# Optimization experiments

Hardware: AMD Instinct MI355X
Metric: run time of the kernel (lower is better)

## Reference

```python
import jax, jax.numpy as jnp
import numpy as np

K = 5            # kernel_size for gaussian and bilateral
PAD = K // 2
SIGMA = 1.0          # gaussian sigma / bilateral sigma_spatial
SIGMA_INT = 0.1      # bilateral sigma_intensity


def _spatial_kernel():
    coords = jnp.arange(K, dtype=jnp.float32) - K // 2
    x, y = jnp.meshgrid(coords, coords, indexing='ij')
    return jnp.exp(-(x ** 2 + y ** 2) / (2.0 * SIGMA ** 2))  # (K, K), unnormalized


def setup_inputs() -> dict:
    key = jax.random.key(0)
    images = jax.random.uniform(key, (8, 3, 512, 512), dtype=jnp.float32)
    return {"images": images}


def _gaussian_filter(images):
    g = _spatial_kernel()
    g = g / g.sum()
    kernel = jnp.tile(g[None, None], (3, 1, 1, 1))  # (3,1,K,K) depthwise
    return jax.lax.conv_general_dilated(
        images, kernel, window_strides=(1, 1),
        padding=[(PAD, PAD), (PAD, PAD)],
        dimension_numbers=('NCHW', 'OIHW', 'NCHW'),
        feature_group_count=3)


def _bilateral_filter(images):
    B, C, H, W = images.shape
    padded = jnp.pad(images, ((0, 0), (0, 0), (PAD, PAD), (PAD, PAD)), mode='reflect')
    # im2col: (B, C, K*K, H, W) -- fixed 25-iteration loop over kernel offsets
    patches = jnp.stack([padded[:, :, i:i + H, j:j + W]
                         for i in range(K) for j in range(K)], axis=2)
    center = patches[:, :, K * K // 2:K * K // 2 + 1]  # (B,C,1,H,W)
    iw = jnp.exp(-(patches - center) ** 2 / (2.0 * SIGMA_INT ** 2))
    sw = _spatial_kernel().reshape(1, 1, K * K, 1, 1)
    w = sw * iw
    w = w / (w.sum(axis=2, keepdims=True) + 1e-8)
    return (patches * w).sum(axis=2)  # (B,C,H,W)


def reference(images):
    # AdaptiveAntiAlias.forward(images, mode='auto')
    gaussian_out = _gaussian_filter(images)
    bilateral_out = _bilateral_filter(images)
    return 0.6 * gaussian_out + 0.4 * bilateral_out
```

## Files before the change

kernel.cpp:

```cpp
#include <hip/hip_runtime.h>

#define IMG_H 512
#define IMG_W 512
#define NCH   24

#if __has_builtin(__builtin_amdgcn_exp2f)
#define EXP2(x) __builtin_amdgcn_exp2f(x)
#else
#define EXP2(x) exp2f(x)
#endif
#if __has_builtin(__builtin_amdgcn_rcpf)
#define RCP(x) __builtin_amdgcn_rcpf(x)
#else
#define RCP(x) (1.0f/(x))
#endif

__device__ __forceinline__ double exs(int r2) {
    switch (r2) {
        case 0: return 1.0;
        case 1: return 0.60653065971263342;
        case 2: return 0.36787944117144233;
        case 4: return 0.13533528323661270;
        case 5: return 0.08208499862389880;
        case 8: return 0.01831563888873418;
    }
    return 0.0;
}

#define SSUM 6.16892408102888092
#define NEG50_LOG2E -72.134752044448169f
#define NEGHALF_LOG2E -0.72134752044448169f

#define XG_INT 126
#define YR_INT 508
#define PER_CH_INT (XG_INT * YR_INT)
#define N_INT (PER_CH_INT * NCH)
#define PER_CH_B (4 * 128 + YR_INT * 2)
#define N_B (PER_CH_B * NCH)

__global__ __launch_bounds__(256) void aa_kernel(const float* __restrict__ in,
                                                 float* __restrict__ out) {
    const int gid = blockIdx.x * 256 + threadIdx.x;

    if (gid < N_INT) {
        const int ch  = gid / PER_CH_INT;
        const int rem = gid - ch * PER_CH_INT;
        const int yy  = rem / XG_INT;
        const int y   = 2 + yy;
        const int x0  = 4 + (rem - yy * XG_INT) * 4;

        const float* __restrict__ img = in + ch * (IMG_H * IMG_W);

        float v[5][8];
        const float* base = img + (y - 2) * IMG_W + (x0 - 2);
        #pragma unroll
        for (int r = 0; r < 5; ++r) {
            const float2* rp = (const float2*)(base + r * IMG_W);
            float2 a = rp[0], b = rp[1], c = rp[2], d = rp[3];
            v[r][0] = a.x; v[r][1] = a.y; v[r][2] = b.x; v[r][3] = b.y;
            v[r][4] = c.x; v[r][5] = c.y; v[r][6] = d.x; v[r][7] = d.y;
        }

        float res[4];
        #pragma unroll
        for (int p = 0; p < 4; ++p) {
            const float ctr = v[2][2 + p];
            float g = 0.f, wsum = 0.f, bsum = 0.f;
            #pragma unroll
            for (int i = 0; i < 5; ++i) {
                #pragma unroll
                for (int j = 0; j < 5; ++j) {
                    const int r2 = (i - 2) * (i - 2) + (j - 2) * (j - 2);
                    const float gk  = (float)(exs(r2) / SSUM);
                    const float lsw = NEGHALF_LOG2E * (float)r2;
                    const float val = v[i][p + j];
                    const float d   = val - ctr;
                    const float w   = EXP2(fmaf(d * d, NEG50_LOG2E, lsw));
                    wsum += w;
                    bsum = fmaf(w, val, bsum);
                    g    = fmaf(gk, val, g);
                }
            }
            res[p] = 0.6f * g + 0.4f * (bsum * RCP(wsum + 1e-8f));
        }

        float4* o4 = (float4*)(out + ch * (IMG_H * IMG_W) + y * IMG_W + x0);
        *o4 = make_float4(res[0], res[1], res[2], res[3]);
    } else {
        const int bi = gid - N_INT;
        const int ch = bi / PER_CH_B;
        const int r  = bi - ch * PER_CH_B;
        int y, x0;
        if (r < 512) {
            const int q = r >> 7;
            y  = (q < 2) ? q : q + 508;
            x0 = (r & 127) << 2;
        } else {
            const int r2_ = r - 512;
            y  = 2 + (r2_ >> 1);
            x0 = (r2_ & 1) ? (IMG_W - 4) : 0;
        }

        const float* __restrict__ img = in + ch * (IMG_H * IMG_W);

        float res[4];
        #pragma unroll
        for (int p = 0; p < 4; ++p) {
            const int x = x0 + p;
            const float ctr = img[y * IMG_W + x];
            float g = 0.f, wsum = 0.f, bsum = 0.f;
            #pragma unroll
            for (int i = 0; i < 5; ++i) {
                const int yy = y + i - 2;
                const bool yin = (yy >= 0) & (yy < IMG_H);
                const int ry = (yy < 0) ? -yy : ((yy >= IMG_H) ? 2 * IMG_H - 2 - yy : yy);
                #pragma unroll
                for (int j = 0; j < 5; ++j) {
                    const int r2 = (i - 2) * (i - 2) + (j - 2) * (j - 2);
                    const float gk  = (float)(exs(r2) / SSUM);
                    const float lsw = NEGHALF_LOG2E * (float)r2;
                    const int xx = x + j - 2;
                    const bool xin = (xx >= 0) & (xx < IMG_W);
                    const int rx = (xx < 0) ? -xx : ((xx >= IMG_W) ? 2 * IMG_W - 2 - xx : xx);
                    const float val = img[ry * IMG_W + rx];
                    const float d   = val - ctr;
                    const float w   = EXP2(fmaf(d * d, NEG50_LOG2E, lsw));
                    wsum += w;
                    bsum = fmaf(w, val, bsum);
                    if (yin & xin) g = fmaf(gk, val, g);
                }
            }
            res[p] = 0.6f * g + 0.4f * (bsum * RCP(wsum + 1e-8f));
        }

        float4* o4 = (float4*)(out + ch * (IMG_H * IMG_W) + y * IMG_W + x0);
        *o4 = make_float4(res[0], res[1], res[2], res[3]);
    }
}

extern "C" void kernel_launch(void* const* d_in, const int* in_sizes, int n_in,
                              void* d_out, int out_size, void* d_ws, size_t ws_size,
                              hipStream_t stream) {
    const float* img = (const float*)d_in[0];
    float* out = (float*)d_out;
    const int total = N_INT + N_B;
    aa_kernel<<<total / 256, 256, 0, stream>>>(img, out);
}
```

Before: 39.36 us.

## Compute two output rows per thread and make the Gaussian separable

Each interior thread now computes a 2x4 output tile from 6 loaded rows instead of a 1x4 tile from 5, so overlapping rows are loaded once and reused. The Gaussian part is split into a vertical column-sum pass and a 5-tap horizontal pass, which cuts its FMAs. The launch bounds also add a minimum-occupancy hint. In exchange, each thread holds more live registers and there are half as many interior threads, which may lower parallelism or cause register spills.

```diff
diff --git a/kernel.cpp b/kernel.cpp
--- a/kernel.cpp
+++ b/kernel.cpp
@@ -4,90 +4,119 @@
 #define IMG_W 512
 #define NCH   24
 
+__device__ __forceinline__ float fexp2(float x) {
 #if __has_builtin(__builtin_amdgcn_exp2f)
-#define EXP2(x) __builtin_amdgcn_exp2f(x)
+    return __builtin_amdgcn_exp2f(x);
 #else
-#define EXP2(x) exp2f(x)
+    float r; asm("v_exp_f32 %0, %1" : "=v"(r) : "v"(x)); return r;
 #endif
+}
+__device__ __forceinline__ float frcp(float x) {
 #if __has_builtin(__builtin_amdgcn_rcpf)
-#define RCP(x) __builtin_amdgcn_rcpf(x)
+    return __builtin_amdgcn_rcpf(x);
 #else
-#define RCP(x) (1.0f/(x))
+    float r; asm("v_rcp_f32 %0, %1" : "=v"(r) : "v"(x)); return r;
 #endif
-
-__device__ __forceinline__ double exs(int r2) {
-    switch (r2) {
-        case 0: return 1.0;
-        case 1: return 0.60653065971263342;
-        case 2: return 0.36787944117144233;
-        case 4: return 0.13533528323661270;
-        case 5: return 0.08208499862389880;
-        case 8: return 0.01831563888873418;
-    }
-    return 0.0;
 }
 
+__device__ __forceinline__ constexpr double exs(int r2) {
+    return (r2 == 0) ? 1.0
+         : (r2 == 1) ? 0.60653065971263342
+         : (r2 == 2) ? 0.36787944117144233
+         : (r2 == 4) ? 0.13533528323661270
+         : (r2 == 5) ? 0.08208499862389880
+         : (r2 == 8) ? 0.01831563888873418 : 0.0;
+}
 #define SSUM 6.16892408102888092
-#define NEG50_LOG2E -72.134752044448169f
-#define NEGHALF_LOG2E -0.72134752044448169f
+__device__ __forceinline__ constexpr float gkc(int r2) { return (float)(exs(r2) / SSUM); }
+__device__ __forceinline__ constexpr float k1(int d)  { return (float)exs(d * d); }
+__device__ __forceinline__ constexpr float k1n(int d) { return (float)(exs(d * d) / SSUM); }
+#define NEG50  -72.134752044448169f
+#define LG     -0.72134752044448169f
 
 #define XG_INT 126
-#define YR_INT 508
-#define PER_CH_INT (XG_INT * YR_INT)
-#define N_INT (PER_CH_INT * NCH)
-#define PER_CH_B (4 * 128 + YR_INT * 2)
+#define YT_INT 254
+#define PER_CH_T (XG_INT * YT_INT)
+#define N_INT (PER_CH_T * NCH)
+#define PER_CH_B (4 * 128 + 508 * 2)
 #define N_B (PER_CH_B * NCH)
+#define N_TOTAL (N_INT + N_B)
 
-__global__ __launch_bounds__(256) void aa_kernel(const float* __restrict__ in,
-                                                 float* __restrict__ out) {
+__global__ __launch_bounds__(256, 4) void aa_kernel(const float* __restrict__ in,
+                                                    float* __restrict__ out) {
     const int gid = blockIdx.x * 256 + threadIdx.x;
 
     if (gid < N_INT) {
-        const int ch  = gid / PER_CH_INT;
-        const int rem = gid - ch * PER_CH_INT;
-        const int yy  = rem / XG_INT;
-        const int y   = 2 + yy;
-        const int x0  = 4 + (rem - yy * XG_INT) * 4;
+        const int ch  = gid / PER_CH_T;
+        const int rem = gid - ch * PER_CH_T;
+        const int ty  = rem / XG_INT;
+        const int y0  = 2 + ty * 2;
+        const int x0  = 4 + (rem - ty * XG_INT) * 4;
 
         const float* __restrict__ img = in + ch * (IMG_H * IMG_W);
+        const float* base = img + (y0 - 2) * IMG_W + (x0 - 2);
 
-        float v[5][8];
-        const float* base = img + (y - 2) * IMG_W + (x0 - 2);
+        float2 L[6][4];
         #pragma unroll
-        for (int r = 0; r < 5; ++r) {
+        for (int r = 0; r < 6; ++r) {
             const float2* rp = (const float2*)(base + r * IMG_W);
-            float2 a = rp[0], b = rp[1], c = rp[2], d = rp[3];
-            v[r][0] = a.x; v[r][1] = a.y; v[r][2] = b.x; v[r][3] = b.y;
-            v[r][4] = c.x; v[r][5] = c.y; v[r][6] = d.x; v[r][7] = d.y;
+            #pragma unroll
+            for (int c = 0; c < 4; ++c) L[r][c] = rp[c];
+        }
+        #define V(r, c) (((c) & 1) ? L[r][(c) >> 1].y : L[r][(c) >> 1].x)
+
+        float cs[2][8];
+        #pragma unroll
+        for (int yr = 0; yr < 2; ++yr) {
+            #pragma unroll
+            for (int c = 0; c < 8; ++c) {
+                float s = k1(2) * V(yr + 0, c);
+                s = fmaf(k1(1), V(yr + 1, c), s);
+                s = fmaf(k1(0), V(yr + 2, c), s);
+                s = fmaf(k1(1), V(yr + 3, c), s);
+                s = fmaf(k1(2), V(yr + 4, c), s);
+                cs[yr][c] = s;
+            }
         }
 
-        float res[4];
+        float res[2][4];
         #pragma unroll
-        for (int p = 0; p < 4; ++p) {
-            const float ctr = v[2][2 + p];
-            float g = 0.f, wsum = 0.f, bsum = 0.f;
+        for (int yr = 0; yr < 2; ++yr) {
             #pragma unroll
-            for (int i = 0; i < 5; ++i) {
+            for (int p = 0; p < 4; ++p) {
+                const float ctr = V(2 + yr, 2 + p);
+                float wsum = 0.f, bsum = 0.f;
                 #pragma unroll
-                for (int j = 0; j < 5; ++j) {
-                    const int r2 = (i - 2) * (i - 2) + (j - 2) * (j - 2);
-                    const float gk  = (float)(exs(r2) / SSUM);
-                    const float lsw = NEGHALF_LOG2E * (float)r2;
-                    const float val = v[i][p + j];
-                    const float d   = val - ctr;
-                    const float w   = EXP2(fmaf(d * d, NEG50_LOG2E, lsw));
-                    wsum += w;
-                    bsum = fmaf(w, val, bsum);
-                    g    = fmaf(gk, val, g);
+                for (int i = 0; i < 5; ++i) {
+                    #pragma unroll
+                    for (int j = 0; j < 5; ++j) {
+                        const int r2 = (i - 2) * (i - 2) + (j - 2) * (j - 2);
+                        const float lsw = LG * (float)r2;
+                        const float val = V(yr + i, p + j);
+                        const float d   = val - ctr;
+                        const float t   = d * d;
+                        const float w   = fexp2(fmaf(t, NEG50, lsw));
+                        wsum += w;
+                        bsum = fmaf(w, val, bsum);
+                    }
                 }
+                float g = k1n(2) * cs[yr][p];
+                g = fmaf(k1n(1), cs[yr][p + 1], g);
+                g = fmaf(k1n(0), cs[yr][p + 2], g);
+                g = fmaf(k1n(1), cs[yr][p + 3], g);
+                g = fmaf(k1n(2), cs[yr][p + 4], g);
+
+                res[yr][p] = fmaf(0.6f, g, 0.4f * (bsum * frcp(wsum + 1e-8f)));
             }
-            res[p] = 0.6f * g + 0.4f * (bsum * RCP(wsum + 1e-8f));
         }
+        #undef V
 
-        float4* o4 = (float4*)(out + ch * (IMG_H * IMG_W) + y * IMG_W + x0);
-        *o4 = make_float4(res[0], res[1], res[2], res[3]);
+        float* op = out + ch * (IMG_H * IMG_W) + y0 * IMG_W + x0;
+        *(float4*)op            = make_float4(res[0][0], res[0][1], res[0][2], res[0][3]);
+        *(float4*)(op + IMG_W)  = make_float4(res[1][0], res[1][1], res[1][2], res[1][3]);
     } else {
         const int bi = gid - N_INT;
+        if (bi >= N_B) return;
         const int ch = bi / PER_CH_B;
         const int r  = bi - ch * PER_CH_B;
         int y, x0;
@@ -117,20 +146,20 @@
                 #pragma unroll
                 for (int j = 0; j < 5; ++j) {
                     const int r2 = (i - 2) * (i - 2) + (j - 2) * (j - 2);
-                    const float gk  = (float)(exs(r2) / SSUM);
-                    const float lsw = NEGHALF_LOG2E * (float)r2;
+                    const float gk  = gkc(r2);
+                    const float lsw = LG * (float)r2;
                     const int xx = x + j - 2;
                     const bool xin = (xx >= 0) & (xx < IMG_W);
                     const int rx = (xx < 0) ? -xx : ((xx >= IMG_W) ? 2 * IMG_W - 2 - xx : xx);
                     const float val = img[ry * IMG_W + rx];
                     const float d   = val - ctr;
-                    const float w   = EXP2(fmaf(d * d, NEG50_LOG2E, lsw));
+                    const float w   = fexp2(fmaf(d * d, NEG50, lsw));
                     wsum += w;
                     bsum = fmaf(w, val, bsum);
                     if (yin & xin) g = fmaf(gk, val, g);
                 }
             }
-            res[p] = 0.6f * g + 0.4f * (bsum * RCP(wsum + 1e-8f));
+            res[p] = fmaf(0.6f, g, 0.4f * (bsum * frcp(wsum + 1e-8f)));
         }
 
         float4* o4 = (float4*)(out + ch * (IMG_H * IMG_W) + y * IMG_W + x0);
@@ -143,6 +172,6 @@
                               hipStream_t stream) {
     const float* img = (const float*)d_in[0];
     float* out = (float*)d_out;
-    const int total = N_INT + N_B;
-    aa_kernel<<<total / 256, 256, 0, stream>>>(img, out);
+    const int blocks = (N_TOTAL + 255) / 256;
+    aa_kernel<<<blocks, 256, 0, stream>>>(img, out);
 }
```

Result: slower. 40.76 us (+3.5%).
